# Kernel tuning notes

Hardware: AMD Instinct MI355X
Metric: run time of the kernel (lower is better)

Reference implementation:

```python
import jax, jax.numpy as jnp
import numpy as np
from jax import lax

NUM_LAYERS = 4
D_MODEL = 768
D_STATE = 128
D_CONV = 4
EXPAND = 2
HEADDIM = 64
D_INNER = EXPAND * D_MODEL            # 1536
NHEADS = D_INNER // HEADDIM           # 24
NGROUPS = 1
CONV_DIM = D_INNER + 2 * NGROUPS * D_STATE        # 1792 (x, B, C go through conv)
D_PROJ = 2 * D_INNER + 2 * NGROUPS * D_STATE + NHEADS  # z, xBC, dt
BATCH, SEQ = 4, 2048


def silu(x):
    return x * jax.nn.sigmoid(x)


def rmsnorm(x, w, eps):
    xf = x.astype(jnp.float32)
    var = jnp.mean(xf * xf, axis=-1, keepdims=True)
    return (w * (xf * lax.rsqrt(var + eps)).astype(x.dtype))


def ssd_scan(xh, dt, A, B, C):
    # xh: (b,s,h,p)  dt: (b,s,h)  A: (h,)  B,C: (b,s,n)
    b = xh.shape[0]
    dA = jnp.exp(dt * A)  # (b,s,h)
    # time-major for scan
    dA_s = dA.transpose(1, 0, 2)          # (s,b,h)
    dt_s = dt.transpose(1, 0, 2)          # (s,b,h)
    x_s = xh.transpose(1, 0, 2, 3)        # (s,b,h,p)
    B_s = B.transpose(1, 0, 2)            # (s,b,n)
    C_s = C.transpose(1, 0, 2)            # (s,b,n)

    h0 = jnp.zeros((b, NHEADS, HEADDIM, D_STATE), xh.dtype)

    def step(h, inp):
        dA_t, dt_t, x_t, B_t, C_t = inp
        # h_t = exp(dt*A) * h_{t-1} + dt * x outer B
        dBx = (dt_t[:, :, None, None] * x_t[:, :, :, None]) * B_t[:, None, None, :]
        h = dA_t[:, :, None, None] * h + dBx
        y = jnp.einsum('bhpn,bn->bhp', h, C_t)
        return h, y

    _, ys = lax.scan(step, h0, (dA_s, dt_s, x_s, B_s, C_s))
    return ys.transpose(1, 0, 2, 3)  # (b,s,h,p)


def mamba2_block(x, Wi, cw, cb, dtb, Alog, Dp, gw, Wo):
    b, s, _ = x.shape
    zxbcdt = jnp.einsum('bsd,ed->bse', x, Wi)  # (b,s,D_PROJ)
    z = zxbcdt[..., :D_INNER]
    xBC = zxbcdt[..., D_INNER:D_INNER + CONV_DIM]
    dt = zxbcdt[..., D_INNER + CONV_DIM:]

    # causal depthwise conv over time on (x,B,C)
    xc = xBC.transpose(0, 2, 1)  # (b, conv_dim, s)
    xc = lax.conv_general_dilated(xc, cw[:, None, :], (1,), [(D_CONV - 1, 0)],
                                  feature_group_count=CONV_DIM)
    xc = xc + cb[None, :, None]
    xBC = silu(xc.transpose(0, 2, 1))

    x_ssm = xBC[..., :D_INNER]
    Bm = xBC[..., D_INNER:D_INNER + D_STATE]
    Cm = xBC[..., D_INNER + D_STATE:]

    dt = jax.nn.softplus(dt + dtb)           # (b,s,h)
    A = -jnp.exp(Alog)                       # (h,)
    xh = x_ssm.reshape(b, s, NHEADS, HEADDIM)

    y = ssd_scan(xh, dt, A, Bm, Cm) + Dp[None, None, :, None] * xh
    y = y.reshape(b, s, D_INNER)
    y = y * silu(z)                          # gated
    y = rmsnorm(y, gw, 1e-5)
    return jnp.einsum('bse,de->bsd', y, Wo)


def setup_inputs() -> dict:
    key = jax.random.key(0)
    ks = jax.random.split(key, 12)
    L = NUM_LAYERS
    sc_in = 1.0 / np.sqrt(D_MODEL)
    sc_out = 1.0 / np.sqrt(D_INNER)
    sc_conv = np.sqrt(2.0 / D_CONV)
    u = jax.random.uniform(ks[5], (L, NHEADS), minval=1e-3, maxval=0.1)
    return {
        'x': jax.random.normal(ks[0], (BATCH, SEQ, D_MODEL), jnp.float32),
        'in_proj_w': jax.random.normal(ks[1], (L, D_PROJ, D_MODEL), jnp.float32) * sc_in,
        'conv_w': jax.random.normal(ks[2], (L, CONV_DIM, D_CONV), jnp.float32) * sc_conv,
        'conv_b': jnp.zeros((L, CONV_DIM), jnp.float32),
        'dt_bias': jnp.log(jnp.expm1(u)),
        'A_log': jnp.log(jax.random.uniform(ks[6], (L, NHEADS), minval=1.0, maxval=16.0)),
        'D_skip': jnp.ones((L, NHEADS), jnp.float32),
        'gnorm_w': jnp.ones((L, D_INNER), jnp.float32),
        'out_proj_w': jax.random.normal(ks[7], (L, D_MODEL, D_INNER), jnp.float32) * sc_out,
        'ln_w': jnp.ones((L, D_MODEL), jnp.float32),
        'final_ln_w': jnp.ones((D_MODEL,), jnp.float32),
    }


def reference(x, in_proj_w, conv_w, conv_b, dt_bias, A_log, D_skip, gnorm_w,
              out_proj_w, ln_w, final_ln_w):
    for l in range(NUM_LAYERS):
        residual = x
        h = rmsnorm(x, ln_w[l], 1e-6)
        h = mamba2_block(h, in_proj_w[l], conv_w[l], conv_b[l], dt_bias[l],
                         A_log[l], D_skip[l], gnorm_w[l], out_proj_w[l])
        x = h + residual
    return rmsnorm(x, final_ln_w, 1e-6)
```

## Files before the change

### kernel.cpp

```cpp
#include <hip/hip_runtime.h>
#include <hip/hip_bf16.h>
#include <math.h>

#define NUM_LAYERS 4
#define D_MODEL 768
#define D_STATE 128
#define D_CONV 4
#define HEADDIM 64
#define D_INNER 1536
#define NHEADS 24
#define CONV_DIM 1792
#define D_PROJ 3352
#define BATCH 4
#define SEQ 2048
#define NROWS (BATCH*SEQ)
#define CHUNK 128
#define NCHUNK (SEQ/CHUNK)
#define LOG2E 1.4426950408889634f

typedef __bf16 bf16x8 __attribute__((ext_vector_type(8)));
typedef float f32x4 __attribute__((ext_vector_type(4)));

#define GLL(gsrc, ldst)                                                        \
  __builtin_amdgcn_global_load_lds(                                            \
      (const __attribute__((address_space(1))) unsigned int*)(gsrc),           \
      (__attribute__((address_space(3))) unsigned int*)(ldst), 16, 0, 0)

__device__ __forceinline__ float warp_reduce_sum(float v) {
  v += __shfl_xor(v, 32);
  v += __shfl_xor(v, 16);
  v += __shfl_xor(v, 8);
  v += __shfl_xor(v, 4);
  v += __shfl_xor(v, 2);
  v += __shfl_xor(v, 1);
  return v;
}

__device__ __forceinline__ float softplusf(float x) {
  return (x > 20.f) ? x : log1pf(expf(x));
}
__device__ __forceinline__ float siluf(float x) {
  return x / (1.f + expf(-x));
}

__device__ __forceinline__ void store_val(float v, float* p) { *p = v; }
__device__ __forceinline__ void store_val(float v, __hip_bfloat16* p) {
  *p = __float2bfloat16(v);
}

__global__ __launch_bounds__(256) void f32_to_bf16_kernel(
    const float* __restrict__ in, __hip_bfloat16* __restrict__ out, size_t n) {
  for (size_t i = ((size_t)blockIdx.x * 256 + threadIdx.x) * 4; i < n;
       i += (size_t)gridDim.x * 256 * 4) {
    float4 v = *(const float4*)(in + i);
    __hip_bfloat16 h0 = __float2bfloat16(v.x), h1 = __float2bfloat16(v.y);
    __hip_bfloat16 h2 = __float2bfloat16(v.z), h3 = __float2bfloat16(v.w);
    ushort4 u;
    u.x = *(unsigned short*)&h0; u.y = *(unsigned short*)&h1;
    u.z = *(unsigned short*)&h2; u.w = *(unsigned short*)&h3;
    *(ushort4*)(out + i) = u;
  }
}

template <typename OUT>
__global__ __launch_bounds__(256) void rmsnorm768_kernel(
    const float* __restrict__ in, const float* __restrict__ w,
    OUT* __restrict__ out, float eps) {
  int row = blockIdx.x;
  const float* x = in + (size_t)row * D_MODEL;
  OUT* o = out + (size_t)row * D_MODEL;
  int t = threadIdx.x;
  float v0 = x[t], v1 = x[t + 256], v2 = x[t + 512];
  float ss = v0 * v0 + v1 * v1 + v2 * v2;
  __shared__ float sred[4];
  ss = warp_reduce_sum(ss);
  if ((t & 63) == 0) sred[t >> 6] = ss;
  __syncthreads();
  float tot = sred[0] + sred[1] + sred[2] + sred[3];
  float inv = rsqrtf(tot / (float)D_MODEL + eps);
  store_val(w[t] * v0 * inv, o + t);
  store_val(w[t + 256] * v1 * inv, o + t + 256);
  store_val(w[t + 512] * v2 * inv, o + t + 512);
}

#define GEMM_PROLOGUE_AND_MAINLOOP(Asrc, Wsrc, Kdim)                           \
  int t = threadIdx.x;                                                         \
  int w = t >> 6, l = t & 63;                                                  \
  int NT = (Kdim) >> 5;                                                        \
  int ldsA0 = (w * 64) * 8;                                                    \
  int ldsA1 = (256 + w * 64) * 8;                                              \
  int lr = l & 15, lk = l >> 4;                                                \
  int wr = w >> 1, wc = w & 1;                                                 \
  int aoff = (lk * 128 + wr * 64 + lr) * 8;                                    \
  int boff = (lk * 128 + wc * 64 + lr) * 8;                                    \
  f32x4 acc[4][4];                                                             \
  _Pragma("unroll") for (int i = 0; i < 4; i++)                                \
      _Pragma("unroll") for (int j = 0; j < 4; j++) acc[i][j] = (f32x4)0.f;    \
  STAGE(0, 0);                                                                 \
  for (int kt = 0; kt < NT; ++kt) {                                            \
    int cur = kt & 1;                                                          \
    if (kt + 1 < NT) {                                                         \
      STAGE(cur ^ 1, (kt + 1) * 32);                                           \
      asm volatile("s_waitcnt vmcnt(4)" ::: "memory");                         \
    } else {                                                                   \
      asm volatile("s_waitcnt vmcnt(0)" ::: "memory");                         \
    }                                                                          \
    __builtin_amdgcn_sched_barrier(0);                                         \
    __builtin_amdgcn_s_barrier();                                              \
    __builtin_amdgcn_sched_barrier(0);                                         \
    bf16x8 av[4], bv[4];                                                       \
    _Pragma("unroll") for (int mi = 0; mi < 4; mi++)                           \
        av[mi] = *(const bf16x8*)&At[cur][aoff + mi * 128];                    \
    _Pragma("unroll") for (int ni = 0; ni < 4; ni++)                           \
        bv[ni] = *(const bf16x8*)&Bt[cur][boff + ni * 128];                    \
    __builtin_amdgcn_s_setprio(1);                                             \
    _Pragma("unroll") for (int mi = 0; mi < 4; mi++)                           \
        _Pragma("unroll") for (int ni = 0; ni < 4; ni++)                       \
            acc[mi][ni] = __builtin_amdgcn_mfma_f32_16x16x32_bf16(             \
                av[mi], bv[ni], acc[mi][ni], 0, 0, 0);                         \
    __builtin_amdgcn_s_setprio(0);                                             \
    __builtin_amdgcn_sched_barrier(0);                                         \
    __builtin_amdgcn_s_barrier();                                              \
  }

#define STAGE(buf, kofs)                                                       \
  do {                                                                         \
    GLL(Aptr + (kofs), &At[buf][ldsA0]);                                       \
    GLL(Aptr + (kofs) + 16, &At[buf][ldsA1]);                                  \
    GLL(Wptr + (kofs), &Bt[buf][ldsA0]);                                       \
    GLL(Wptr + (kofs) + 16, &Bt[buf][ldsA1]);                                  \
  } while (0)

__global__ __launch_bounds__(256) void gemm_bf16_kernel(
    const __hip_bfloat16* __restrict__ A, const __hip_bfloat16* __restrict__ W,
    const float* __restrict__ res, float* __restrict__ C,
    int M, int N, int K) {
  __shared__ __bf16 At[2][4096];
  __shared__ __bf16 Bt[2][4096];
  int cpx = gridDim.x >> 3;
  int bid = blockIdx.x;
  int bid2 = (bid & 7) * cpx + (bid >> 3);
  int nbn = (N + 127) >> 7;
  int bn = bid2 % nbn;
  int bm = bid2 / nbn;
  int m0 = bm * 128, n0 = bn * 128;
  int srow = threadIdx.x & 127;
  int kbase = (threadIdx.x >> 7) * 8;
  const __hip_bfloat16* Aptr = A + (size_t)(m0 + srow) * K + kbase;
  int nrow = n0 + srow; if (nrow >= N) nrow = N - 1;
  const __hip_bfloat16* Wptr = W + (size_t)nrow * K + kbase;

  GEMM_PROLOGUE_AND_MAINLOOP(A, W, K)

  int rbase = (l >> 4) * 4;
#pragma unroll
  for (int ni = 0; ni < 4; ni++) {
    int n = n0 + wc * 64 + ni * 16 + (l & 15);
    if (n >= N) continue;
#pragma unroll
    for (int mi = 0; mi < 4; mi++) {
#pragma unroll
      for (int r = 0; r < 4; r++) {
        int m = m0 + wr * 64 + mi * 16 + rbase + r;
        float v = acc[mi][ni][r];
        if (res) v += res[(size_t)m * N + n];
        C[(size_t)m * N + n] = v;
      }
    }
  }
}

__global__ __launch_bounds__(512, 2) void gemm_inproj_kernel(
    const __hip_bfloat16* __restrict__ A, const __hip_bfloat16* __restrict__ W,
    __hip_bfloat16* __restrict__ zout, __hip_bfloat16* __restrict__ xout,
    float* __restrict__ dtout) {
  const int K = D_MODEL, N = D_PROJ;
  __shared__ __bf16 At[2][16384];
  __shared__ __bf16 Bt[2][16384];
  int cpx = gridDim.x >> 3;
  int bid = blockIdx.x;
  int bid2 = (bid & 7) * cpx + (bid >> 3);
  int bn = bid2 % 14;
  int bm = bid2 / 14;
  int m0 = bm * 256, n0 = bn * 256;
  int t = threadIdx.x;
  int w = t >> 6, l = t & 63;
  int lr = l & 15, lk = l >> 4;
  int wr = w >> 2, wc = w & 3;

  int srow = t & 255;
  int shi = t >> 8;
  const __hip_bfloat16* Arow = A + (size_t)(m0 + srow) * K;
  int nrow = n0 + srow; if (nrow >= N) nrow = N - 1;
  const __hip_bfloat16* Wrow = W + (size_t)nrow * K;

#define STAGE3(buf, kt)                                                       \
  do {                                                                        \
    _Pragma("unroll") for (int i = 0; i < 4; i++) {                           \
      int oct = 2 * i + shi;                                                  \
      GLL(Arow + (kt) * 64 + oct * 8, &At[buf][(oct * 256 + srow) * 8]);      \
    }                                                                         \
    _Pragma("unroll") for (int i = 0; i < 4; i++) {                           \
      int oct = 2 * i + shi;                                                  \
      GLL(Wrow + (kt) * 64 + oct * 8, &Bt[buf][(oct * 256 + srow) * 8]);      \
    }                                                                         \
  } while (0)

  f32x4 acc[8][4];
#pragma unroll
  for (int i = 0; i < 8; i++)
#pragma unroll
    for (int j = 0; j < 4; j++) acc[i][j] = (f32x4)0.f;

  const int NT = 12;
  STAGE3(0, 0);
  for (int kt = 0; kt < NT; ++kt) {
    int cur = kt & 1;
    if (kt + 1 < NT) {
      STAGE3(cur ^ 1, kt + 1);
      asm volatile("s_waitcnt vmcnt(8)" ::: "memory");
    } else {
      asm volatile("s_waitcnt vmcnt(0)" ::: "memory");
    }
    __builtin_amdgcn_sched_barrier(0);
    __builtin_amdgcn_s_barrier();
    __builtin_amdgcn_sched_barrier(0);
#pragma unroll
    for (int ks = 0; ks < 2; ks++) {
      int ko = ks * 4 + lk;
      bf16x8 av[8], bv[4];
#pragma unroll
      for (int mi = 0; mi < 8; mi++)
        av[mi] = *(const bf16x8*)&At[cur][(ko * 256 + wr * 128 + mi * 16 + lr) * 8];
#pragma unroll
      for (int ni = 0; ni < 4; ni++)
        bv[ni] = *(const bf16x8*)&Bt[cur][(ko * 256 + wc * 64 + ni * 16 + lr) * 8];
      __builtin_amdgcn_s_setprio(1);
#pragma unroll
      for (int mi = 0; mi < 8; mi++)
#pragma unroll
        for (int ni = 0; ni < 4; ni++)
          acc[mi][ni] = __builtin_amdgcn_mfma_f32_16x16x32_bf16(
              av[mi], bv[ni], acc[mi][ni], 0, 0, 0);
      __builtin_amdgcn_s_setprio(0);
    }
    __builtin_amdgcn_sched_barrier(0);
    __builtin_amdgcn_s_barrier();
  }
#undef STAGE3

  int rbase = lk * 4;
  if (bn < 6) {
#pragma unroll
    for (int ni = 0; ni < 4; ni++) {
      int n = n0 + wc * 64 + ni * 16 + lr;
#pragma unroll
      for (int mi = 0; mi < 8; mi++)
#pragma unroll
        for (int r = 0; r < 4; r++) {
          int m = m0 + wr * 128 + mi * 16 + rbase + r;
          zout[(size_t)m * D_INNER + n] = __float2bfloat16(acc[mi][ni][r]);
        }
    }
  } else if (bn < 13) {
    int nb = n0 - D_INNER;
#pragma unroll
    for (int ni = 0; ni < 4; ni++) {
      int n = nb + wc * 64 + ni * 16 + lr;
#pragma unroll
      for (int mi = 0; mi < 8; mi++)
#pragma unroll
        for (int r = 0; r < 4; r++) {
          int m = m0 + wr * 128 + mi * 16 + rbase + r;
          xout[(size_t)m * CONV_DIM + n] = __float2bfloat16(acc[mi][ni][r]);
        }
    }
  } else {
#pragma unroll
    for (int ni = 0; ni < 4; ni++) {
      int loc = wc * 64 + ni * 16 + lr;
      if (loc >= 24) continue;
#pragma unroll
      for (int mi = 0; mi < 8; mi++)
#pragma unroll
        for (int r = 0; r < 4; r++) {
          int m = m0 + wr * 128 + mi * 16 + rbase + r;
          dtout[(size_t)m * 24 + loc] = acc[mi][ni][r];
        }
    }
  }
}

__global__ __launch_bounds__(128) void dt_kernel(
    const float* __restrict__ dtraw, const float* __restrict__ dt_bias,
    const float* __restrict__ A_log, float* __restrict__ dtbuf,
    float* __restrict__ cum2buf) {
  int c = blockIdx.x & 15;
  int h = (blockIdx.x >> 4) % NHEADS;
  int b = blockIdx.x / (16 * NHEADS);
  int t = threadIdx.x;
  int s = c * CHUNK + t;
  float Ah = -expf(A_log[h]);
  float raw = dtraw[((size_t)b * SEQ + s) * 24 + h] + dt_bias[h];
  float dt = softplusf(raw);
  __shared__ float sc[128];
  sc[t] = dt * Ah;
  __syncthreads();
  for (int off = 1; off < 128; off <<= 1) {
    float v = (t >= off) ? sc[t - off] : 0.f;
    __syncthreads();
    sc[t] += v;
    __syncthreads();
  }
  size_t o = ((size_t)b * NHEADS + h) * SEQ + s;
  dtbuf[o] = dt;
  cum2buf[o] = sc[t] * LOG2E;
}

__global__ __launch_bounds__(256) void conv_tiles_kernel(
    const __hip_bfloat16* __restrict__ xbc, const float* __restrict__ cw,
    const float* __restrict__ cb, __hip_bfloat16* __restrict__ xA,
    __hip_bfloat16* __restrict__ Bkt, __hip_bfloat16* __restrict__ Bkn,
    __hip_bfloat16* __restrict__ Ckn) {
  __shared__ float srows[11 * CONV_DIM];
  int to = blockIdx.x & 15;
  int c  = (blockIdx.x >> 4) & 15;
  int b  = blockIdx.x >> 8;
  int t  = threadIdx.x;
  int sb = c * CHUNK + to * 8;
  const __hip_bfloat16* base = xbc + (size_t)b * SEQ * CONV_DIM;
  for (int e = t; e < 11 * 224; e += 256) {
    int r = e / 224, c8 = (e - r * 224) * 8;
    int s = sb - 3 + r;
    float* dst = &srows[r * CONV_DIM + c8];
    if (s >= 0) {
      bf16x8 v = *(const bf16x8*)&base[(size_t)s * CONV_DIM + c8];
#pragma unroll
      for (int j = 0; j < 8; j++) dst[j] = (float)v[j];
    } else {
#pragma unroll
      for (int j = 0; j < 8; j++) dst[j] = 0.f;
    }
  }
  __syncthreads();
  int bc = b * 16 + c;
#pragma unroll
  for (int k7 = 0; k7 < 7; k7++) {
    int ch = t + k7 * 256;
    float w0 = cw[ch * 4], w1 = cw[ch * 4 + 1];
    float w2 = cw[ch * 4 + 2], w3 = cw[ch * 4 + 3];
    float bias = cb[ch];
    float out[8];
#pragma unroll
    for (int j = 0; j < 8; j++) {
      float a = bias;
      a = fmaf(srows[(j + 0) * CONV_DIM + ch], w0, a);
      a = fmaf(srows[(j + 1) * CONV_DIM + ch], w1, a);
      a = fmaf(srows[(j + 2) * CONV_DIM + ch], w2, a);
      a = fmaf(srows[(j + 3) * CONV_DIM + ch], w3, a);
      out[j] = siluf(a);
    }
    if (ch < D_INNER) {
      int h = ch >> 6, p = ch & 63;
      bf16x8 v;
#pragma unroll
      for (int j = 0; j < 8; j++) v[j] = (__bf16)out[j];
      *(bf16x8*)&xA[((((size_t)bc * 24 + h) * 16 + to) * 64 + p) * 8] = v;
    } else if (ch < D_INNER + D_STATE) {
      int n = ch - D_INNER;
      bf16x8 v;
#pragma unroll
      for (int j = 0; j < 8; j++) v[j] = (__bf16)out[j];
      *(bf16x8*)&Bkt[(((size_t)bc * 16 + to) * 128 + n) * 8] = v;
      __hip_bfloat16* dst = Bkn + (size_t)bc * 16384 + ((n >> 3) * 128) * 8 + (n & 7);
#pragma unroll
      for (int j = 0; j < 8; j++)
        dst[(to * 8 + j) * 8] = __float2bfloat16(out[j]);
    } else {
      int n = ch - D_INNER - D_STATE;
      __hip_bfloat16* dst = Ckn + (size_t)bc * 16384 + ((n >> 3) * 128) * 8 + (n & 7);
#pragma unroll
      for (int j = 0; j < 8; j++)
        dst[(to * 8 + j) * 8] = __float2bfloat16(out[j]);
    }
  }
}

__global__ __launch_bounds__(256) void ssd_state_kernel(
    const __hip_bfloat16* __restrict__ xA, const __hip_bfloat16* __restrict__ Bkt,
    const float* __restrict__ dtbuf, const float* __restrict__ cum2buf,
    __hip_bfloat16* __restrict__ states) {
  __shared__ __bf16 sX[8192];
  __shared__ __bf16 sB[16384];
  __shared__ float swdt[128];
  int c = blockIdx.x & 15;
  int h = (blockIdx.x >> 4) % NHEADS;
  int b = blockIdx.x / (16 * NHEADS);
  int t = threadIdx.x;
  int l = t & 63, w = t >> 6;
  const __hip_bfloat16* xsrc = xA + ((size_t)(b * 16 + c) * 24 + h) * 8192;
  const __hip_bfloat16* bsrc = Bkt + (size_t)(b * 16 + c) * 16384;
#pragma unroll
  for (int i = 0; i < 4; i++) GLL(xsrc + (i * 256 + t) * 8, &sX[(i * 256 + t) * 8]);
#pragma unroll
  for (int i = 0; i < 8; i++) GLL(bsrc + (i * 256 + t) * 8, &sB[(i * 256 + t) * 8]);
  {
    size_t dto = ((size_t)b * NHEADS + h) * SEQ + c * CHUNK;
    if (t < 128) {
      float total2 = cum2buf[dto + 127];
      swdt[t] = dtbuf[dto + t] * exp2f(total2 - cum2buf[dto + t]);
    }
  }
  __syncthreads();
#pragma unroll
  for (int i = 0; i < 4; i++) {
    int o = i * 256 + t;
    int to = o >> 6;
    bf16x8 v = *(bf16x8*)&sX[o * 8];
#pragma unroll
    for (int j = 0; j < 8; j++)
      v[j] = (__bf16)((float)v[j] * swdt[to * 8 + j]);
    *(bf16x8*)&sX[o * 8] = v;
  }
  __syncthreads();
  int n0w = w * 32;
  f32x4 acc[4][2];
#pragma unroll
  for (int i = 0; i < 4; i++)
#pragma unroll
    for (int j = 0; j < 2; j++) acc[i][j] = (f32x4)0.f;
#pragma unroll
  for (int kk = 0; kk < 4; kk++) {
    int ko = kk * 4 + (l >> 4);
    bf16x8 av[4], bv[2];
#pragma unroll
    for (int mi = 0; mi < 4; mi++)
      av[mi] = *(const bf16x8*)&sX[(ko * 64 + mi * 16 + (l & 15)) * 8];
#pragma unroll
    for (int ni = 0; ni < 2; ni++)
      bv[ni] = *(const bf16x8*)&sB[(ko * 128 + n0w + ni * 16 + (l & 15)) * 8];
#pragma unroll
    for (int mi = 0; mi < 4; mi++)
#pragma unroll
      for (int ni = 0; ni < 2; ni++)
        acc[mi][ni] = __builtin_amdgcn_mfma_f32_16x16x32_bf16(
            av[mi], bv[ni], acc[mi][ni], 0, 0, 0);
  }
  __hip_bfloat16* dst = states + (((size_t)b * NHEADS + h) * 16 + c) * 8192;
#pragma unroll
  for (int mi = 0; mi < 4; mi++)
#pragma unroll
    for (int ni = 0; ni < 2; ni++) {
      int n = n0w + ni * 16 + (l & 15);
#pragma unroll
      for (int r = 0; r < 4; r++) {
        int p = mi * 16 + (l >> 4) * 4 + r;
        dst[((n >> 3) * 64 + p) * 8 + (n & 7)] = __float2bfloat16(acc[mi][ni][r]);
      }
    }
}

__global__ __launch_bounds__(256) void ssd_chunkscan_kernel(
    __hip_bfloat16* __restrict__ states, const float* __restrict__ cum2buf) {
  int q = blockIdx.x & 3;
  int bh = blockIdx.x >> 2;
  int t = threadIdx.x;
  int o = q * 256 + t;
  __hip_bfloat16* base = states + (size_t)bh * NCHUNK * 8192 + (size_t)o * 8;
  const float* c2 = cum2buf + (size_t)bh * SEQ;
  float hacc[8];
#pragma unroll
  for (int j = 0; j < 8; j++) hacc[j] = 0.f;
  for (int c = 0; c < NCHUNK; c++) {
    float eA = exp2f(c2[c * 128 + 127]);
    __hip_bfloat16* p = base + (size_t)c * 8192;
    bf16x8 v = *(bf16x8*)p;
    bf16x8 wv;
#pragma unroll
    for (int j = 0; j < 8; j++) {
      float tmp = (float)v[j];
      wv[j] = (__bf16)hacc[j];
      hacc[j] = fmaf(eA, hacc[j], tmp);
    }
    *(bf16x8*)p = wv;
  }
}

__global__ __launch_bounds__(256) void ssd_output_kernel(
    const __hip_bfloat16* __restrict__ Ckn, const __hip_bfloat16* __restrict__ Bkn,
    const __hip_bfloat16* __restrict__ xA, const __hip_bfloat16* __restrict__ states,
    const float* __restrict__ dtbuf, const float* __restrict__ cum2buf,
    const float* __restrict__ D_skip, __hip_bfloat16* __restrict__ y) {
  __shared__ __bf16 sC[16384];
  __shared__ __bf16 sBS[16384];
  __shared__ __bf16 sXH[8192];
  int c = blockIdx.x & 15;
  int h = (blockIdx.x >> 4) % NHEADS;
  int b = blockIdx.x / (16 * NHEADS);
  int t = threadIdx.x;
  int l = t & 63, w = t >> 6;
  int bc = b * 16 + c;
  const __hip_bfloat16* csrc = Ckn + (size_t)bc * 16384;
  const __hip_bfloat16* bsrc = Bkn + (size_t)bc * 16384;
  const __hip_bfloat16* xsrc = xA + ((size_t)bc * 24 + h) * 8192;
#pragma unroll
  for (int i = 0; i < 8; i++) GLL(csrc + (i * 256 + t) * 8, &sC[(i * 256 + t) * 8]);
#pragma unroll
  for (int i = 0; i < 8; i++) GLL(bsrc + (i * 256 + t) * 8, &sBS[(i * 256 + t) * 8]);
#pragma unroll
  for (int i = 0; i < 4; i++) GLL(xsrc + (i * 256 + t) * 8, &sXH[(i * 256 + t) * 8]);

  size_t dto = ((size_t)b * NHEADS + h) * SEQ + c * CHUNK;
  float cum2_t[8], cum2_tau[8], dt_tau[8];
#pragma unroll
  for (int fm = 0; fm < 2; fm++)
#pragma unroll
    for (int r = 0; r < 4; r++)
      cum2_t[fm * 4 + r] = cum2buf[dto + w * 32 + fm * 16 + (l >> 4) * 4 + r];
#pragma unroll
  for (int fc = 0; fc < 8; fc++) {
    cum2_tau[fc] = cum2buf[dto + fc * 16 + (l & 15)];
    dt_tau[fc] = dtbuf[dto + fc * 16 + (l & 15)];
  }
  float Dh = D_skip[h];
  __syncthreads();

  f32x4 g[2][8];
#pragma unroll
  for (int i = 0; i < 2; i++)
#pragma unroll
    for (int j = 0; j < 8; j++) g[i][j] = (f32x4)0.f;
#pragma unroll
  for (int kk = 0; kk < 4; kk++) {
    int ko = kk * 4 + (l >> 4);
    bf16x8 a0 = *(const bf16x8*)&sC[(ko * 128 + w * 32 + (l & 15)) * 8];
    bf16x8 a1 = *(const bf16x8*)&sC[(ko * 128 + w * 32 + 16 + (l & 15)) * 8];
#pragma unroll
    for (int fc = 0; fc < 8; fc++) {
      bf16x8 bv = *(const bf16x8*)&sBS[(ko * 128 + fc * 16 + (l & 15)) * 8];
      g[0][fc] = __builtin_amdgcn_mfma_f32_16x16x32_bf16(a0, bv, g[0][fc], 0, 0, 0);
      g[1][fc] = __builtin_amdgcn_mfma_f32_16x16x32_bf16(a1, bv, g[1][fc], 0, 0, 0);
    }
  }
  __syncthreads();

#pragma unroll
  for (int fm = 0; fm < 2; fm++)
#pragma unroll
    for (int fc = 0; fc < 8; fc++) {
      int tau = fc * 16 + (l & 15);
#pragma unroll
      for (int r = 0; r < 4; r++) {
        int tt = w * 32 + fm * 16 + (l >> 4) * 4 + r;
        float v = 0.f;
        if (tt >= tau) {
          v = exp2f(cum2_t[fm * 4 + r] - cum2_tau[fc]) * dt_tau[fc] * g[fm][fc][r];
          if (tt == tau) v += Dh;
        }
        sBS[((tau >> 3) * 128 + tt) * 8 + (tau & 7)] = (__bf16)v;
      }
    }
  f32x4 y1[2][4];
#pragma unroll
  for (int i = 0; i < 2; i++)
#pragma unroll
    for (int j = 0; j < 4; j++) y1[i][j] = (f32x4)0.f;
#pragma unroll
  for (int kk = 0; kk < 4; kk++) {
    int ko = kk * 4 + (l >> 4);
    bf16x8 a0 = *(const bf16x8*)&sBS[(ko * 128 + w * 32 + (l & 15)) * 8];
    bf16x8 a1 = *(const bf16x8*)&sBS[(ko * 128 + w * 32 + 16 + (l & 15)) * 8];
#pragma unroll
    for (int fc = 0; fc < 4; fc++) {
      bf16x8 bv = *(const bf16x8*)&sXH[(ko * 64 + fc * 16 + (l & 15)) * 8];
      y1[0][fc] = __builtin_amdgcn_mfma_f32_16x16x32_bf16(a0, bv, y1[0][fc], 0, 0, 0);
      y1[1][fc] = __builtin_amdgcn_mfma_f32_16x16x32_bf16(a1, bv, y1[1][fc], 0, 0, 0);
    }
  }
  __syncthreads();
  const __hip_bfloat16* hsrc = states + (((size_t)b * NHEADS + h) * 16 + c) * 8192;
#pragma unroll
  for (int i = 0; i < 4; i++) GLL(hsrc + (i * 256 + t) * 8, &sXH[(i * 256 + t) * 8]);
  __syncthreads();

  f32x4 y2[2][4];
#pragma unroll
  for (int i = 0; i < 2; i++)
#pragma unroll
    for (int j = 0; j < 4; j++) y2[i][j] = (f32x4)0.f;
#pragma unroll
  for (int kk = 0; kk < 4; kk++) {
    int ko = kk * 4 + (l >> 4);
    bf16x8 a0 = *(const bf16x8*)&sC[(ko * 128 + w * 32 + (l & 15)) * 8];
    bf16x8 a1 = *(const bf16x8*)&sC[(ko * 128 + w * 32 + 16 + (l & 15)) * 8];
#pragma unroll
    for (int fc = 0; fc < 4; fc++) {
      bf16x8 bv = *(const bf16x8*)&sXH[(ko * 64 + fc * 16 + (l & 15)) * 8];
      y2[0][fc] = __builtin_amdgcn_mfma_f32_16x16x32_bf16(a0, bv, y2[0][fc], 0, 0, 0);
      y2[1][fc] = __builtin_amdgcn_mfma_f32_16x16x32_bf16(a1, bv, y2[1][fc], 0, 0, 0);
    }
  }

  __hip_bfloat16* yr = y + ((size_t)b * SEQ + c * CHUNK) * D_INNER + h * 64;
#pragma unroll
  for (int fm = 0; fm < 2; fm++)
#pragma unroll
    for (int r = 0; r < 4; r++) {
      int tt = w * 32 + fm * 16 + (l >> 4) * 4 + r;
      float sdec = exp2f(cum2_t[fm * 4 + r]);
#pragma unroll
      for (int fc = 0; fc < 4; fc++) {
        int p = fc * 16 + (l & 15);
        yr[(size_t)tt * D_INNER + p] =
            __float2bfloat16(y1[fm][fc][r] + sdec * y2[fm][fc][r]);
      }
    }
}

__global__ __launch_bounds__(192) void gate_norm_kernel(
    __hip_bfloat16* __restrict__ y, const __hip_bfloat16* __restrict__ z,
    const float* __restrict__ gw) {
  int row = blockIdx.x;
  const __hip_bfloat16* zr = z + (size_t)row * D_INNER;
  __hip_bfloat16* yr = y + (size_t)row * D_INNER;
  int t = threadIdx.x;
  bf16x8 yv = *(const bf16x8*)&yr[t * 8];
  bf16x8 zv = *(const bf16x8*)&zr[t * 8];
  float vals[8];
  float ss = 0.f;
#pragma unroll
  for (int j = 0; j < 8; j++) {
    float zf = (float)zv[j];
    float v = (float)yv[j] * siluf(zf);
    vals[j] = v;
    ss += v * v;
  }
  __shared__ float sred[3];
  ss = warp_reduce_sum(ss);
  if ((t & 63) == 0) sred[t >> 6] = ss;
  __syncthreads();
  float tot = sred[0] + sred[1] + sred[2];
  float inv = rsqrtf(tot / (float)D_INNER + 1e-5f);
  bf16x8 o;
#pragma unroll
  for (int j = 0; j < 8; j++)
    o[j] = (__bf16)(gw[t * 8 + j] * vals[j] * inv);
  *(bf16x8*)&yr[t * 8] = o;
}

extern "C" void kernel_launch(void* const* d_in, const int* in_sizes, int n_in,
                              void* d_out, int out_size, void* d_ws, size_t ws_size,
                              hipStream_t stream) {
  const float* x          = (const float*)d_in[0];
  const float* in_proj_w  = (const float*)d_in[1];
  const float* conv_w     = (const float*)d_in[2];
  const float* conv_b     = (const float*)d_in[3];
  const float* dt_bias    = (const float*)d_in[4];
  const float* A_log      = (const float*)d_in[5];
  const float* D_skip     = (const float*)d_in[6];
  const float* gnorm_w    = (const float*)d_in[7];
  const float* out_proj_w = (const float*)d_in[8];
  const float* ln_w       = (const float*)d_in[9];
  const float* final_ln_w = (const float*)d_in[10];

  float* ws = (float*)d_ws;
  float* curx   = ws; ws += (size_t)NROWS * D_MODEL;
  float* dtraw  = ws; ws += (size_t)NROWS * 24;
  float* dtbuf  = ws; ws += (size_t)BATCH * NHEADS * SEQ;
  float* cum2   = ws; ws += (size_t)BATCH * NHEADS * SEQ;
  __hip_bfloat16* zbuf   = (__hip_bfloat16*)ws; ws += (size_t)NROWS * D_INNER / 2;
  __hip_bfloat16* xbcbuf = (__hip_bfloat16*)ws; ws += (size_t)NROWS * CONV_DIM / 2;
  __hip_bfloat16* hbuf_b = (__hip_bfloat16*)ws; ws += (size_t)NROWS * D_MODEL / 2;
  __hip_bfloat16* ybuf_b = (__hip_bfloat16*)ws; ws += (size_t)NROWS * D_INNER / 2;
  __hip_bfloat16* wi_b   = (__hip_bfloat16*)ws; ws += (size_t)NUM_LAYERS * D_PROJ * D_MODEL / 2;
  __hip_bfloat16* wo_b   = (__hip_bfloat16*)ws; ws += (size_t)NUM_LAYERS * D_MODEL * D_INNER / 2;
  __hip_bfloat16* xAb    = (__hip_bfloat16*)ws; ws += (size_t)BATCH * NCHUNK * 24 * 8192 / 2;
  __hip_bfloat16* Bkt    = (__hip_bfloat16*)ws; ws += (size_t)BATCH * NCHUNK * 16384 / 2;
  __hip_bfloat16* Bkn    = (__hip_bfloat16*)ws; ws += (size_t)BATCH * NCHUNK * 16384 / 2;
  __hip_bfloat16* Ckn    = (__hip_bfloat16*)ws; ws += (size_t)BATCH * NCHUNK * 16384 / 2;
  __hip_bfloat16* states = (__hip_bfloat16*)ws;

  f32_to_bf16_kernel<<<1024, 256, 0, stream>>>(
      in_proj_w, wi_b, (size_t)NUM_LAYERS * D_PROJ * D_MODEL);
  f32_to_bf16_kernel<<<1024, 256, 0, stream>>>(
      out_proj_w, wo_b, (size_t)NUM_LAYERS * D_MODEL * D_INNER);

  for (int l = 0; l < NUM_LAYERS; l++) {
    const float* xin = (l == 0) ? x : curx;
    rmsnorm768_kernel<__hip_bfloat16><<<NROWS, 256, 0, stream>>>(
        xin, ln_w + (size_t)l * D_MODEL, hbuf_b, 1e-6f);

    gemm_inproj_kernel<<<448, 512, 0, stream>>>(
        hbuf_b, wi_b + (size_t)l * D_PROJ * D_MODEL, zbuf, xbcbuf, dtraw);

    dt_kernel<<<BATCH * NHEADS * NCHUNK, 128, 0, stream>>>(
        dtraw, dt_bias + l * NHEADS, A_log + l * NHEADS, dtbuf, cum2);

    conv_tiles_kernel<<<BATCH * NCHUNK * 16, 256, 0, stream>>>(
        xbcbuf, conv_w + (size_t)l * CONV_DIM * D_CONV,
        conv_b + (size_t)l * CONV_DIM, xAb, Bkt, Bkn, Ckn);

    ssd_state_kernel<<<BATCH * NHEADS * NCHUNK, 256, 0, stream>>>(
        xAb, Bkt, dtbuf, cum2, states);

    ssd_chunkscan_kernel<<<BATCH * NHEADS * 4, 256, 0, stream>>>(states, cum2);

    ssd_output_kernel<<<BATCH * NHEADS * NCHUNK, 256, 0, stream>>>(
        Ckn, Bkn, xAb, states, dtbuf, cum2, D_skip + l * NHEADS, ybuf_b);

    gate_norm_kernel<<<NROWS, 192, 0, stream>>>(
        ybuf_b, zbuf, gnorm_w + (size_t)l * D_INNER);

    gemm_bf16_kernel<<<64 * 6, 256, 0, stream>>>(
        ybuf_b, wo_b + (size_t)l * D_MODEL * D_INNER, xin, curx,
        NROWS, D_MODEL, D_INNER);
  }
  rmsnorm768_kernel<float><<<NROWS, 256, 0, stream>>>(
      curx, final_ln_w, (float*)d_out, 1e-6f);
}
```

Baseline: 1.069 ms.

## Split in-proj GEMM k-step into four quadrant phases with staggered A/B prefetch

Restructures the in-projection GEMM main loop into four MFMA phases over quadrants of the 256x256 tile, separated by block barriers. Next-tile A and B loads are issued after different phase barriers, so each buffer is refilled once its last reader has finished. The change lowers launch bounds to one block per CU so more registers are available for the split fragment arrays. It adds barriers per k-step, waits on vmcnt(0) at the top of each step, and loses the occupancy that let a second block hide latency.

```diff
diff --git a/kernel.cpp b/kernel.cpp
--- a/kernel.cpp
+++ b/kernel.cpp
@@ -170,7 +170,7 @@
   }
 }
 
-__global__ __launch_bounds__(512, 2) void gemm_inproj_kernel(
+__global__ __launch_bounds__(512, 1) void gemm_inproj_kernel(
     const __hip_bfloat16* __restrict__ A, const __hip_bfloat16* __restrict__ W,
     __hip_bfloat16* __restrict__ zout, __hip_bfloat16* __restrict__ xout,
     float* __restrict__ dtout) {
@@ -194,17 +194,26 @@
   int nrow = n0 + srow; if (nrow >= N) nrow = N - 1;
   const __hip_bfloat16* Wrow = W + (size_t)nrow * K;
 
-#define STAGE3(buf, kt)                                                       \
+#define STAGE_A(buf, kt)                                                      \
   do {                                                                        \
     _Pragma("unroll") for (int i = 0; i < 4; i++) {                           \
       int oct = 2 * i + shi;                                                  \
       GLL(Arow + (kt) * 64 + oct * 8, &At[buf][(oct * 256 + srow) * 8]);      \
     }                                                                         \
+  } while (0)
+#define STAGE_B(buf, kt)                                                      \
+  do {                                                                        \
     _Pragma("unroll") for (int i = 0; i < 4; i++) {                           \
       int oct = 2 * i + shi;                                                  \
       GLL(Wrow + (kt) * 64 + oct * 8, &Bt[buf][(oct * 256 + srow) * 8]);      \
     }                                                                         \
   } while (0)
+#define PH_BAR()                                                              \
+  do {                                                                        \
+    __builtin_amdgcn_sched_barrier(0);                                        \
+    __builtin_amdgcn_s_barrier();                                             \
+    __builtin_amdgcn_sched_barrier(0);                                        \
+  } while (0)
 
   f32x4 acc[8][4];
 #pragma unroll
@@ -213,41 +222,88 @@
     for (int j = 0; j < 4; j++) acc[i][j] = (f32x4)0.f;
 
   const int NT = 12;
-  STAGE3(0, 0);
+  STAGE_A(0, 0);
+  STAGE_B(0, 0);
   for (int kt = 0; kt < NT; ++kt) {
     int cur = kt & 1;
-    if (kt + 1 < NT) {
-      STAGE3(cur ^ 1, kt + 1);
-      asm volatile("s_waitcnt vmcnt(8)" ::: "memory");
-    } else {
-      asm volatile("s_waitcnt vmcnt(0)" ::: "memory");
-    }
-    __builtin_amdgcn_sched_barrier(0);
-    __builtin_amdgcn_s_barrier();
-    __builtin_amdgcn_sched_barrier(0);
+    asm volatile("s_waitcnt vmcnt(0)" ::: "memory");
+    PH_BAR();
+    if (kt + 1 < NT) STAGE_A(cur ^ 1, kt + 1);
+    bf16x8 av0[4][2], bv0[2][2];
 #pragma unroll
     for (int ks = 0; ks < 2; ks++) {
       int ko = ks * 4 + lk;
-      bf16x8 av[8], bv[4];
-#pragma unroll
-      for (int mi = 0; mi < 8; mi++)
-        av[mi] = *(const bf16x8*)&At[cur][(ko * 256 + wr * 128 + mi * 16 + lr) * 8];
-#pragma unroll
-      for (int ni = 0; ni < 4; ni++)
-        bv[ni] = *(const bf16x8*)&Bt[cur][(ko * 256 + wc * 64 + ni * 16 + lr) * 8];
-      __builtin_amdgcn_s_setprio(1);
-#pragma unroll
-      for (int mi = 0; mi < 8; mi++)
-#pragma unroll
-        for (int ni = 0; ni < 4; ni++)
+#pragma unroll
+      for (int mi = 0; mi < 4; mi++)
+        av0[mi][ks] = *(const bf16x8*)&At[cur][(ko * 256 + wr * 128 + mi * 16 + lr) * 8];
+#pragma unroll
+      for (int ni = 0; ni < 2; ni++)
+        bv0[ni][ks] = *(const bf16x8*)&Bt[cur][(ko * 256 + wc * 64 + ni * 16 + lr) * 8];
+    }
+    __builtin_amdgcn_s_setprio(1);
+#pragma unroll
+    for (int ks = 0; ks < 2; ks++)
+#pragma unroll
+      for (int mi = 0; mi < 4; mi++)
+#pragma unroll
+        for (int ni = 0; ni < 2; ni++)
           acc[mi][ni] = __builtin_amdgcn_mfma_f32_16x16x32_bf16(
-              av[mi], bv[ni], acc[mi][ni], 0, 0, 0);
-      __builtin_amdgcn_s_setprio(0);
-    }
-    __builtin_amdgcn_sched_barrier(0);
-    __builtin_amdgcn_s_barrier();
-  }
-#undef STAGE3
+              av0[mi][ks], bv0[ni][ks], acc[mi][ni], 0, 0, 0);
+    __builtin_amdgcn_s_setprio(0);
+    PH_BAR();
+    if (kt + 1 < NT) STAGE_B(cur ^ 1, kt + 1);
+    bf16x8 bv1[2][2];
+#pragma unroll
+    for (int ks = 0; ks < 2; ks++) {
+      int ko = ks * 4 + lk;
+#pragma unroll
+      for (int ni = 0; ni < 2; ni++)
+        bv1[ni][ks] = *(const bf16x8*)&Bt[cur][(ko * 256 + wc * 64 + (ni + 2) * 16 + lr) * 8];
+    }
+    __builtin_amdgcn_s_setprio(1);
+#pragma unroll
+    for (int ks = 0; ks < 2; ks++)
+#pragma unroll
+      for (int mi = 0; mi < 4; mi++)
+#pragma unroll
+        for (int ni = 0; ni < 2; ni++)
+          acc[mi][ni + 2] = __builtin_amdgcn_mfma_f32_16x16x32_bf16(
+              av0[mi][ks], bv1[ni][ks], acc[mi][ni + 2], 0, 0, 0);
+    __builtin_amdgcn_s_setprio(0);
+    PH_BAR();
+    bf16x8 av1[4][2];
+#pragma unroll
+    for (int ks = 0; ks < 2; ks++) {
+      int ko = ks * 4 + lk;
+#pragma unroll
+      for (int mi = 0; mi < 4; mi++)
+        av1[mi][ks] = *(const bf16x8*)&At[cur][(ko * 256 + wr * 128 + (mi + 4) * 16 + lr) * 8];
+    }
+    __builtin_amdgcn_s_setprio(1);
+#pragma unroll
+    for (int ks = 0; ks < 2; ks++)
+#pragma unroll
+      for (int mi = 0; mi < 4; mi++)
+#pragma unroll
+        for (int ni = 0; ni < 2; ni++)
+          acc[mi + 4][ni + 2] = __builtin_amdgcn_mfma_f32_16x16x32_bf16(
+              av1[mi][ks], bv1[ni][ks], acc[mi + 4][ni + 2], 0, 0, 0);
+    __builtin_amdgcn_s_setprio(0);
+    PH_BAR();
+    __builtin_amdgcn_s_setprio(1);
+#pragma unroll
+    for (int ks = 0; ks < 2; ks++)
+#pragma unroll
+      for (int mi = 0; mi < 4; mi++)
+#pragma unroll
+        for (int ni = 0; ni < 2; ni++)
+          acc[mi + 4][ni] = __builtin_amdgcn_mfma_f32_16x16x32_bf16(
+              av1[mi][ks], bv0[ni][ks], acc[mi + 4][ni], 0, 0, 0);
+    __builtin_amdgcn_s_setprio(0);
+  }
+#undef STAGE_A
+#undef STAGE_B
+#undef PH_BAR
 
   int rbase = lk * 4;
   if (bn < 6) {
```

New measurement: 1.086 ms. About the same (+1.6%).
